# Kernel optimization log

Hardware: AMD Instinct MI355X
Metric: run time of the kernel (lower is better)

The kernel has to match this reference:

```python
import jax, jax.numpy as jnp
import numpy as np

N, E, F, H, O = 50000, 1_600_000, 512, 256, 128


def setup_inputs() -> dict:
    key = jax.random.key(0)
    k1, k2, k3, k4, k5 = jax.random.split(key, 5)
    x = jax.random.normal(k1, (N, F), dtype=jnp.float32)
    edge_index = jax.random.randint(k2, (2, E), 0, N, dtype=jnp.int32)
    edge_weight = jax.random.uniform(k3, (E,), dtype=jnp.float32)
    W1 = jax.random.normal(k4, (F, H), dtype=jnp.float32) * (1.0 / np.sqrt(F))
    b1 = jnp.zeros((H,), dtype=jnp.float32)
    W2 = jax.random.normal(k5, (H, O), dtype=jnp.float32) * (1.0 / np.sqrt(H))
    b2 = jnp.zeros((O,), dtype=jnp.float32)
    return {"x": x, "edge_index": edge_index, "edge_weight": edge_weight,
            "W1": W1, "b1": b1, "W2": W2, "b2": b2}


def reference(x, edge_index, edge_weight, W1, b1, W2, b2):
    n = x.shape[0]
    src, dst = edge_index[0], edge_index[1]
    # GCNConv: add self-loops with weight 1
    loop = jnp.arange(n, dtype=src.dtype)
    src = jnp.concatenate([src, loop])
    dst = jnp.concatenate([dst, loop])
    w = jnp.concatenate([edge_weight, jnp.ones((n,), dtype=x.dtype)])
    # symmetric normalization D^{-1/2} (A+I) D^{-1/2}
    deg = jax.ops.segment_sum(w, dst, num_segments=n)
    dinv = jnp.where(deg > 0, jax.lax.rsqrt(deg), 0.0)
    norm = dinv[src] * w * dinv[dst]  # [E+N]

    def conv(h, W, b):
        h = h @ W                                   # linear first (PyG GCNConv)
        msg = h[src] * norm[:, None]                # gather + scale per edge
        return jax.ops.segment_sum(msg, dst, num_segments=n) + b

    h = jax.nn.relu(conv(x, W1, b1))
    return conv(h, W2, b2)
```

## Files before the change

### kernel.cpp

```cpp
#include <hip/hip_runtime.h>
#include <hip/hip_bf16.h>

#define CAP 80
#define NPB 98
#define BCAP 4096
#define CHUNK_E 2048

typedef __attribute__((ext_vector_type(8))) short bf16x8;
typedef __attribute__((ext_vector_type(4))) float f32x4;
typedef __attribute__((ext_vector_type(2))) float f32x2;

__device__ inline ushort f2bf(float f){
  union{float f; unsigned u;} c{f};
  unsigned r = (c.u + 0x7fff + ((c.u>>16)&1)) >> 16;
  return (ushort)r;
}
__device__ inline float blo(unsigned u){ return __uint_as_float(u<<16); }
__device__ inline float bhi(unsigned u){ return __uint_as_float(u & 0xffff0000u); }


__device__ inline unsigned char fp8_enc(float v){
#if __has_builtin(__builtin_amdgcn_cvt_pk_fp8_f32)
  int p = __builtin_amdgcn_cvt_pk_fp8_f32(v, v, 0, false);
  return (unsigned char)(p & 0xff);
#else
  unsigned s = v < 0.f ? 0x80u : 0u;
  float a = fabsf(v);
  if (a >= 448.f) return (unsigned char)(s | 0x7Eu);
  if (a < 7.8125e-3f){
    int m = (int)rintf(a * 512.f); if (m > 15) m = 15;
    if (m >= 8) return (unsigned char)(s | (1u<<3) | (unsigned)(m-8));
    return (unsigned char)(s | (unsigned)m);
  }
  int e; float fr = frexpf(a, &e);
  int m = (int)rintf(fr * 16.f);
  if (m == 16){ m = 8; e++; }
  int ee = e - 1 + 7;
  if (ee > 15) return (unsigned char)(s | 0x7Eu);
  return (unsigned char)(s | (unsigned)(ee<<3) | (unsigned)(m-8));
#endif
}

__device__ inline void fp8x4_dec(unsigned w, float d[4]){
#if __has_builtin(__builtin_amdgcn_cvt_pk_f32_fp8)
  f32x2 lo = __builtin_amdgcn_cvt_pk_f32_fp8((int)w, false);
  f32x2 hi = __builtin_amdgcn_cvt_pk_f32_fp8((int)w, true);
  d[0] = lo[0]; d[1] = lo[1]; d[2] = hi[0]; d[3] = hi[1];
#else
  #pragma unroll
  for (int i = 0; i < 4; ++i){
    unsigned v = (w >> (8*i)) & 0xffu;
    unsigned s = v & 0x80u, e = (v>>3)&15u, m = v&7u;
    float f = e ? ldexpf((float)(8+m), (int)e - 10) : ldexpf((float)m, -9);
    d[i] = s ? -f : f;
  }
#endif
}


__global__ void k_wconv(const float* __restrict__ Wm, ushort* __restrict__ Wt, int K, int D){
  int idx = blockIdx.x*blockDim.x + threadIdx.x;
  if (idx < D*K){
    int d = idx / K, k = idx - d*K;
    Wt[idx] = f2bf(Wm[(size_t)k*D + d]);
  }
}


__global__ __launch_bounds__(256) void k_bin(const int* __restrict__ src,
                                             const int* __restrict__ dst,
                                             const float* __restrict__ w,
                                             int* __restrict__ bktcur,
                                             uint2* __restrict__ bkt, int E, int nb){
  __shared__ int hist[512];
  __shared__ int base[512];
  const int t  = threadIdx.x;
  const int c0 = blockIdx.x * CHUNK_E;
  const int cend = min(c0 + CHUNK_E, E);
  for (int i = t; i < nb; i += 256) hist[i] = 0;
  __syncthreads();
  const bool full = ((cend - c0) == CHUNK_E) && ((E & 3) == 0);
  int4 d4[2], s4[2]; float4 w4[2];
  if (full){
    const int e0 = c0 + t*8;
    #pragma unroll
    for (int q = 0; q < 2; ++q){
      d4[q] = *(const int4*)(dst + e0 + q*4);
      s4[q] = *(const int4*)(src + e0 + q*4);
      w4[q] = *(const float4*)(w  + e0 + q*4);
    }
    #pragma unroll
    for (int q = 0; q < 2; ++q){
      atomicAdd(&hist[d4[q].x/NPB],1); atomicAdd(&hist[d4[q].y/NPB],1);
      atomicAdd(&hist[d4[q].z/NPB],1); atomicAdd(&hist[d4[q].w/NPB],1);
    }
  } else {
    for (int e = c0 + t; e < cend; e += 256)
      atomicAdd(&hist[dst[e]/NPB], 1);
  }
  __syncthreads();
  for (int i = t; i < nb; i += 256){
    int h = hist[i];
    base[i] = (h > 0) ? atomicAdd(&bktcur[i], h) : 0;
    hist[i] = 0;
  }
  __syncthreads();
  if (full){
    #pragma unroll
    for (int q = 0; q < 2; ++q){
      int   dd[4] = {d4[q].x, d4[q].y, d4[q].z, d4[q].w};
      int   ss[4] = {s4[q].x, s4[q].y, s4[q].z, s4[q].w};
      float ww[4] = {w4[q].x, w4[q].y, w4[q].z, w4[q].w};
      #pragma unroll
      for (int j = 0; j < 4; ++j){
        int b = dd[j] / NPB;
        int pos = base[b] + atomicAdd(&hist[b], 1);
        if (pos < BCAP){
          unsigned lo = ((unsigned)ss[j] << 16) | (unsigned)f2bf(ww[j]);
          bkt[(size_t)b*BCAP + pos] = make_uint2(lo, (unsigned)dd[j]);
        }
      }
    }
  } else {
    for (int e = c0 + t; e < cend; e += 256){
      int d = dst[e];
      int b = d / NPB;
      int pos = base[b] + atomicAdd(&hist[b], 1);
      if (pos < BCAP){
        unsigned lo = ((unsigned)src[e] << 16) | (unsigned)f2bf(w[e]);
        bkt[(size_t)b*BCAP + pos] = make_uint2(lo, (unsigned)d);
      }
    }
  }
}


__global__ __launch_bounds__(256) void k_build(const uint2* __restrict__ bkt,
                                               const int* __restrict__ bktcur,
                                               unsigned* __restrict__ padcsr,
                                               int* __restrict__ cnt,
                                               float* __restrict__ dinv, int N){
  __shared__ unsigned rows[NPB][CAP];
  __shared__ int   lcnt[NPB];
  __shared__ float lws[NPB];
  const int b = blockIdx.x;
  const int t = threadIdx.x;
  const int node0 = b * NPB;
  for (int i = t; i < NPB; i += 256){ lcnt[i] = 0; lws[i] = 0.f; }
  __syncthreads();
  const int cb = min(bktcur[b], BCAP);
  for (int e = t; e < cb; e += 256){
    uint2 rec = bkt[(size_t)b*BCAP + e];
    int ld = (int)rec.y - node0;
    int pos = atomicAdd(&lcnt[ld], 1);
    if (pos < CAP) rows[ld][pos] = rec.x;
    atomicAdd(&lws[ld], blo(rec.x));
  }
  __syncthreads();
  const int maxn = min(NPB, N - node0);
  unsigned* gslice = padcsr + (size_t)node0*CAP;
  const int tot = maxn * CAP;
  const unsigned* lbase = &rows[0][0];
  for (int i = t*4; i < tot; i += 1024)
    *(uint4*)(gslice + i) = *(const uint4*)(lbase + i);
  for (int i = t; i < maxn; i += 256){
    cnt[node0 + i]  = lcnt[i];
    dinv[node0 + i] = rsqrtf(1.f + lws[i]);
  }
}


__global__ __launch_bounds__(256, 3) void gemm1_f8(const float* __restrict__ X,
                                                   const ushort* __restrict__ Wt,
                                                   unsigned char* __restrict__ out, int M){
  __shared__ short As[128][56];
  __shared__ short Bs[256][56];
  const int t    = threadIdx.x;
  const int lane = t & 63;
  const int wave = t >> 6;
  const int wr   = wave >> 1;
  const int wc   = wave & 1;
  const int i0   = blockIdx.x * 128;

  f32x4 acc[4][8];
  #pragma unroll
  for (int m = 0; m < 4; ++m)
    #pragma unroll
    for (int nn = 0; nn < 8; ++nn)
      acc[m][nn] = (f32x4){0.f,0.f,0.f,0.f};

  const int arow = t >> 1;
  const int akh  = (t & 1) * 16;

  for (int kt = 0; kt < 512; kt += 32){
    {
      int gi = i0 + arow;
      ushort hv[16];
      if (gi < M){
        const float4* ap4 = (const float4*)(X + (size_t)gi*512 + kt + akh);
        #pragma unroll
        for (int q = 0; q < 4; ++q){
          float4 v = ap4[q];
          hv[q*4+0] = f2bf(v.x); hv[q*4+1] = f2bf(v.y);
          hv[q*4+2] = f2bf(v.z); hv[q*4+3] = f2bf(v.w);
        }
      } else {
        #pragma unroll
        for (int q = 0; q < 16; ++q) hv[q] = 0;
      }
      *(uint4*)&As[arow][akh]     = *(uint4*)&hv[0];
      *(uint4*)&As[arow][akh + 8] = *(uint4*)&hv[8];
    }
    {
      const ushort* wp = Wt + (size_t)t*512 + kt;
      *(uint4*)&Bs[t][0]  = *(const uint4*)wp;
      *(uint4*)&Bs[t][8]  = *(const uint4*)(wp + 8);
      *(uint4*)&Bs[t][16] = *(const uint4*)(wp + 16);
      *(uint4*)&Bs[t][24] = *(const uint4*)(wp + 24);
    }
    __syncthreads();
    bf16x8 a_f[4], b_f[8];
    #pragma unroll
    for (int m = 0; m < 4; ++m)
      a_f[m] = *(bf16x8*)&As[wr*64 + m*16 + (lane & 15)][(lane >> 4) * 8];
    #pragma unroll
    for (int nn = 0; nn < 8; ++nn)
      b_f[nn] = *(bf16x8*)&Bs[wc*128 + nn*16 + (lane & 15)][(lane >> 4) * 8];
    #pragma unroll
    for (int m = 0; m < 4; ++m)
      #pragma unroll
      for (int nn = 0; nn < 8; ++nn)
        acc[m][nn] = __builtin_amdgcn_mfma_f32_16x16x32_bf16(a_f[m], b_f[nn], acc[m][nn], 0, 0, 0);
    __syncthreads();
  }
  #pragma unroll
  for (int m = 0; m < 4; ++m){
    int r_base = i0 + wr*64 + m*16 + ((lane >> 4) << 2);
    #pragma unroll
    for (int nn = 0; nn < 8; ++nn){
      int c = wc*128 + nn*16 + (lane & 15);
      #pragma unroll
      for (int r = 0; r < 4; ++r){
        int gr = r_base + r;
        if (gr < M) out[(size_t)gr*256 + c] = fp8_enc(acc[m][nn][r]);
      }
    }
  }
}


__global__ __launch_bounds__(256, 2) void gemm2_bf(const ushort* __restrict__ X,
                                                   const ushort* __restrict__ Wt,
                                                   ushort* __restrict__ out, int M){
  constexpr int K = 256, DOUT = 128;
  __shared__ short As[128][56];
  __shared__ short Bs[128][56];
  const int t    = threadIdx.x;
  const int lane = t & 63;
  const int wave = t >> 6;
  const int wr   = wave >> 1;
  const int wc   = wave & 1;
  const int i0   = blockIdx.x * 128;

  f32x4 acc[4][4];
  #pragma unroll
  for (int m = 0; m < 4; ++m)
    #pragma unroll
    for (int nn = 0; nn < 4; ++nn)
      acc[m][nn] = (f32x4){0.f,0.f,0.f,0.f};

  const int arow = t >> 1;
  const int akh  = (t & 1) * 16;

  for (int kt = 0; kt < K; kt += 32){
    {
      int gi = i0 + arow;
      ushort hv[16];
      if (gi < M){
        const uint4* ap4 = (const uint4*)(X + (size_t)gi*K + kt + akh);
        uint4 u0 = ap4[0], u1 = ap4[1];
        *(uint4*)&hv[0] = u0; *(uint4*)&hv[8] = u1;
      } else {
        #pragma unroll
        for (int q = 0; q < 16; ++q) hv[q] = 0;
      }
      *(uint4*)&As[arow][akh]     = *(uint4*)&hv[0];
      *(uint4*)&As[arow][akh + 8] = *(uint4*)&hv[8];
    }
    {
      int bn = t & 127;
      int kh = (t >> 7) * 16;
      const ushort* wp = Wt + (size_t)bn*K + kt + kh;
      *(uint4*)&Bs[bn][kh]     = *(const uint4*)wp;
      *(uint4*)&Bs[bn][kh + 8] = *(const uint4*)(wp + 8);
    }
    __syncthreads();
    bf16x8 a_f[4], b_f[4];
    #pragma unroll
    for (int m = 0; m < 4; ++m)
      a_f[m] = *(bf16x8*)&As[wr*64 + m*16 + (lane & 15)][(lane >> 4) * 8];
    #pragma unroll
    for (int nn = 0; nn < 4; ++nn)
      b_f[nn] = *(bf16x8*)&Bs[wc*64 + nn*16 + (lane & 15)][(lane >> 4) * 8];
    #pragma unroll
    for (int m = 0; m < 4; ++m)
      #pragma unroll
      for (int nn = 0; nn < 4; ++nn)
        acc[m][nn] = __builtin_amdgcn_mfma_f32_16x16x32_bf16(a_f[m], b_f[nn], acc[m][nn], 0, 0, 0);
    __syncthreads();
  }
  #pragma unroll
  for (int m = 0; m < 4; ++m){
    int r_base = i0 + wr*64 + m*16 + ((lane >> 4) << 2);
    #pragma unroll
    for (int nn = 0; nn < 4; ++nn){
      int c = wc*64 + nn*16 + (lane & 15);
      #pragma unroll
      for (int r = 0; r < 4; ++r){
        int gr = r_base + r;
        if (gr < M) out[(size_t)gr*DOUT + c] = f2bf(acc[m][nn][r]);
      }
    }
  }
}


__global__ __launch_bounds__(64) void agg_fp8(const unsigned char* __restrict__ tin,
                                              const int* __restrict__ cnt,
                                              const unsigned* __restrict__ padcsr,
                                              const float* __restrict__ dinv,
                                              const float* __restrict__ bias,
                                              ushort* __restrict__ outp, int n){
  constexpr int U = 4;
  int node = blockIdx.x;
  if (node >= n) return;
  int lane = threadIdx.x & 63;
  int sl   = lane & 15;
  int part = lane >> 4;
  const size_t boff = (size_t)sl * 16;
  const unsigned* row = padcsr + (size_t)node*CAP;

  float acc[16];
  #pragma unroll
  for (int i = 0; i < 16; ++i) acc[i] = 0.f;
  int len = min(cnt[node], CAP);
  int e = 0;
  for (; e + 4*U <= len; e += 4*U){
    int srcs[U]; float ws[U];
    #pragma unroll
    for (int u = 0; u < U; ++u){
      unsigned rec = row[e + u*4 + part];
      srcs[u] = (int)(rec >> 16); ws[u] = blo(rec);
    }
    float dv[U];
    #pragma unroll
    for (int u = 0; u < U; ++u) dv[u] = dinv[srcs[u]];
    uint4 g[U];
    #pragma unroll
    for (int u = 0; u < U; ++u) g[u] = *(const uint4*)(tin + (size_t)srcs[u]*256 + boff);
    #pragma unroll
    for (int u = 0; u < U; ++u){
      float w = ws[u] * dv[u];
      float d[4];
      fp8x4_dec(g[u].x, d);
      acc[0]  += d[0]*w; acc[1]  += d[1]*w; acc[2]  += d[2]*w; acc[3]  += d[3]*w;
      fp8x4_dec(g[u].y, d);
      acc[4]  += d[0]*w; acc[5]  += d[1]*w; acc[6]  += d[2]*w; acc[7]  += d[3]*w;
      fp8x4_dec(g[u].z, d);
      acc[8]  += d[0]*w; acc[9]  += d[1]*w; acc[10] += d[2]*w; acc[11] += d[3]*w;
      fp8x4_dec(g[u].w, d);
      acc[12] += d[0]*w; acc[13] += d[1]*w; acc[14] += d[2]*w; acc[15] += d[3]*w;
    }
  }
  for (; e < len; e += 4){
    int idx = e + part;
    int s = node; float w = 0.f;
    if (idx < len){ unsigned rec = row[idx]; s = (int)(rec >> 16); w = blo(rec) * dinv[s]; }
    uint4 g = *(const uint4*)(tin + (size_t)s*256 + boff);
    float d[4];
    fp8x4_dec(g.x, d);
    acc[0]  += d[0]*w; acc[1]  += d[1]*w; acc[2]  += d[2]*w; acc[3]  += d[3]*w;
    fp8x4_dec(g.y, d);
    acc[4]  += d[0]*w; acc[5]  += d[1]*w; acc[6]  += d[2]*w; acc[7]  += d[3]*w;
    fp8x4_dec(g.z, d);
    acc[8]  += d[0]*w; acc[9]  += d[1]*w; acc[10] += d[2]*w; acc[11] += d[3]*w;
    fp8x4_dec(g.w, d);
    acc[12] += d[0]*w; acc[13] += d[1]*w; acc[14] += d[2]*w; acc[15] += d[3]*w;
  }
  #pragma unroll
  for (int i = 0; i < 16; ++i){
    acc[i] += __shfl_xor(acc[i], 16);
    acc[i] += __shfl_xor(acc[i], 32);
  }
  if (part == 0){
    float di = dinv[node];
    uint4 gs = *(const uint4*)(tin + (size_t)node*256 + boff);
    float d[4];
    fp8x4_dec(gs.x, d);
    acc[0]  += d[0]*di; acc[1]  += d[1]*di; acc[2]  += d[2]*di; acc[3]  += d[3]*di;
    fp8x4_dec(gs.y, d);
    acc[4]  += d[0]*di; acc[5]  += d[1]*di; acc[6]  += d[2]*di; acc[7]  += d[3]*di;
    fp8x4_dec(gs.z, d);
    acc[8]  += d[0]*di; acc[9]  += d[1]*di; acc[10] += d[2]*di; acc[11] += d[3]*di;
    fp8x4_dec(gs.w, d);
    acc[12] += d[0]*di; acc[13] += d[1]*di; acc[14] += d[2]*di; acc[15] += d[3]*di;
    ushort hv[16];
    #pragma unroll
    for (int q = 0; q < 4; ++q){
      float4 bq = *(const float4*)(bias + sl*16 + q*4);
      acc[q*4+0] = acc[q*4+0]*di + bq.x;
      acc[q*4+1] = acc[q*4+1]*di + bq.y;
      acc[q*4+2] = acc[q*4+2]*di + bq.z;
      acc[q*4+3] = acc[q*4+3]*di + bq.w;
    }
    #pragma unroll
    for (int i = 0; i < 16; ++i) hv[i] = f2bf(fmaxf(acc[i], 0.f));
    ushort* op = outp + (size_t)node*256 + sl*16;
    *(uint4*)op       = *(uint4*)&hv[0];
    *(uint4*)(op + 8) = *(uint4*)&hv[8];
  }
}


template<int D, int MODE>
__global__ __launch_bounds__(64) void agg_pad(const ushort* __restrict__ tin,
                                              const int* __restrict__ cnt,
                                              const unsigned* __restrict__ padcsr,
                                              const float* __restrict__ dinv,
                                              const float* __restrict__ bias,
                                              void* __restrict__ outp, int n){
  constexpr int LPR = D/8;
  constexpr int EPW = 64/LPR;
  constexpr int U   = 4;
  int node = blockIdx.x;
  if (node >= n) return;
  int lane = threadIdx.x & 63;
  int sl   = lane & (LPR-1);
  int part = lane / LPR;
  const size_t boff = (size_t)sl*8;
  const unsigned* row = padcsr + (size_t)node*CAP;

  float acc[8] = {0,0,0,0,0,0,0,0};
  int len = min(cnt[node], CAP);
  int e = 0;
  for (; e + EPW*U <= len; e += EPW*U){
    int srcs[U]; float ws[U];
    #pragma unroll
    for (int u = 0; u < U; ++u){
      unsigned rec = row[e + u*EPW + part];
      srcs[u] = (int)(rec >> 16); ws[u] = blo(rec);
    }
    float dv[U];
    #pragma unroll
    for (int u = 0; u < U; ++u) dv[u] = dinv[srcs[u]];
    uint4 g[U];
    #pragma unroll
    for (int u = 0; u < U; ++u) g[u] = *(const uint4*)(tin + (size_t)srcs[u]*D + boff);
    #pragma unroll
    for (int u = 0; u < U; ++u){
      float w = ws[u] * dv[u];
      acc[0] += blo(g[u].x)*w; acc[1] += bhi(g[u].x)*w;
      acc[2] += blo(g[u].y)*w; acc[3] += bhi(g[u].y)*w;
      acc[4] += blo(g[u].z)*w; acc[5] += bhi(g[u].z)*w;
      acc[6] += blo(g[u].w)*w; acc[7] += bhi(g[u].w)*w;
    }
  }
  for (; e < len; e += EPW){
    int idx = e + part;
    int s = node; float w = 0.f;
    if (idx < len){
      unsigned rec = row[idx];
      s = (int)(rec >> 16);
      w = blo(rec) * dinv[s];
    }
    uint4 g = *(const uint4*)(tin + (size_t)s*D + boff);
    acc[0] += blo(g.x)*w; acc[1] += bhi(g.x)*w;
    acc[2] += blo(g.y)*w; acc[3] += bhi(g.y)*w;
    acc[4] += blo(g.z)*w; acc[5] += bhi(g.z)*w;
    acc[6] += blo(g.w)*w; acc[7] += bhi(g.w)*w;
  }
  #pragma unroll
  for (int i = 0; i < 8; ++i){
    if constexpr (EPW == 4) acc[i] += __shfl_xor(acc[i], 16);
    acc[i] += __shfl_xor(acc[i], 32);
  }
  if (part == 0){
    float di = dinv[node];
    uint4 gs = *(const uint4*)(tin + (size_t)node*D + boff);
    acc[0] += blo(gs.x)*di; acc[1] += bhi(gs.x)*di;
    acc[2] += blo(gs.y)*di; acc[3] += bhi(gs.y)*di;
    acc[4] += blo(gs.z)*di; acc[5] += bhi(gs.z)*di;
    acc[6] += blo(gs.w)*di; acc[7] += bhi(gs.w)*di;
    float4 b0 = *(const float4*)(bias + sl*8);
    float4 b1 = *(const float4*)(bias + sl*8 + 4);
    acc[0] = acc[0]*di + b0.x; acc[1] = acc[1]*di + b0.y;
    acc[2] = acc[2]*di + b0.z; acc[3] = acc[3]*di + b0.w;
    acc[4] = acc[4]*di + b1.x; acc[5] = acc[5]*di + b1.y;
    acc[6] = acc[6]*di + b1.z; acc[7] = acc[7]*di + b1.w;
    if constexpr (MODE == 0){
      ushort hv[8];
      #pragma unroll
      for (int i = 0; i < 8; ++i) hv[i] = f2bf(fmaxf(acc[i], 0.f));
      *(uint4*)((ushort*)outp + (size_t)node*D + boff) = *(uint4*)&hv[0];
    } else {
      float* op = (float*)outp + (size_t)node*D + boff;
      *(float4*)op     = make_float4(acc[0],acc[1],acc[2],acc[3]);
      *(float4*)(op+4) = make_float4(acc[4],acc[5],acc[6],acc[7]);
    }
  }
}


static inline size_t align_up(size_t x){ return (x + 255) & ~(size_t)255; }

extern "C" void kernel_launch(void* const* d_in, const int* in_sizes, int n_in,
                              void* d_out, int out_size, void* d_ws, size_t ws_size,
                              hipStream_t stream){
  const float* x   = (const float*)d_in[0];
  const int*   ei  = (const int*)  d_in[1];
  const float* ew  = (const float*)d_in[2];
  const float* W1  = (const float*)d_in[3];
  const float* b1  = (const float*)d_in[4];
  const float* W2  = (const float*)d_in[5];
  const float* b2  = (const float*)d_in[6];

  const int H = in_sizes[4];
  const int F = in_sizes[3] / H;
  const int N = in_sizes[0] / F;
  const int E = in_sizes[2];
  const int O = in_sizes[6];

  const int* src = ei;
  const int* dst = ei + E;

  const int nb = (N + NPB - 1) / NPB;

  char* p = (char*)d_ws;
  int*      cnt     = (int*)p;            p += align_up((size_t)N*4);
  float*    dinv    = (float*)p;          p += align_up((size_t)N*4);
  int*      bktcur  = (int*)p;            p += align_up((size_t)nb*4);
  ushort*   Wt1     = (ushort*)p;         p += align_up((size_t)H*F*2);
  ushort*   Wt2     = (ushort*)p;         p += align_up((size_t)O*H*2);
  unsigned* padcsr  = (unsigned*)p;       p += align_up((size_t)N*CAP*4);
  unsigned char* t1 = (unsigned char*)p;  p += align_up((size_t)N*H);
  uint2*    bkt     = (uint2*)p;
  ushort*   h1      = (ushort*)p;         p += align_up((size_t)N*H*2 > (size_t)nb*BCAP*8 ?
                                                        (size_t)N*H*2 : (size_t)nb*BCAP*8);
  ushort*   t2      = (ushort*)t1;

  hipLaunchKernelGGL(k_wconv, dim3((H*F+255)/256), dim3(256), 0, stream, W1, Wt1, F, H);
  hipLaunchKernelGGL(k_wconv, dim3((O*H+255)/256), dim3(256), 0, stream, W2, Wt2, H, O);

  hipMemsetAsync(bktcur, 0, (size_t)nb*4, stream);
  hipLaunchKernelGGL(k_bin, dim3((E+CHUNK_E-1)/CHUNK_E), dim3(256), 0, stream,
                     src, dst, ew, bktcur, bkt, E, nb);
  hipLaunchKernelGGL(k_build, dim3(nb), dim3(256), 0, stream,
                     bkt, bktcur, padcsr, cnt, dinv, N);

  hipLaunchKernelGGL(gemm1_f8, dim3((N+127)/128), dim3(256), 0, stream, x, Wt1, t1, N);
  hipLaunchKernelGGL(agg_fp8, dim3(N), dim3(64), 0, stream,
                     t1, cnt, padcsr, dinv, b1, h1, N);

  hipLaunchKernelGGL(gemm2_bf, dim3((N+127)/128), dim3(256), 0, stream, h1, Wt2, t2, N);
  hipLaunchKernelGGL((agg_pad<128,1>), dim3(N), dim3(64), 0, stream,
                     t2, cnt, padcsr, dinv, b2, d_out, N);
}
```

Measured before the change: 235.5 us.

## Merge weight conversion into binning kernel and shrink GEMM row tiles to 64

Folds the two weight-transpose/bf16 conversion launches into the edge-binning kernel as extra leading blocks, removing two kernel launches. Both GEMMs move from 128-row to 64-row tiles with fewer accumulators per wave and higher launch-bounds occupancy, giving more blocks across the GPU for N=50000. The B-tile load in gemm1 is staggered to reduce LDS bank conflicts. Smaller tiles reload the weight tile more often per output row, which raises global and LDS traffic.

```diff
diff --git a/kernel.cpp b/kernel.cpp
--- a/kernel.cpp
+++ b/kernel.cpp
@@ -58,24 +58,32 @@
 }
 
 
-__global__ void k_wconv(const float* __restrict__ Wm, ushort* __restrict__ Wt, int K, int D){
-  int idx = blockIdx.x*blockDim.x + threadIdx.x;
-  if (idx < D*K){
-    int d = idx / K, k = idx - d*K;
-    Wt[idx] = f2bf(Wm[(size_t)k*D + d]);
-  }
-}
-
-
-__global__ __launch_bounds__(256) void k_bin(const int* __restrict__ src,
-                                             const int* __restrict__ dst,
+__global__ __launch_bounds__(256) void k_pre(const float* __restrict__ W1, ushort* __restrict__ Wt1,
+                                             const float* __restrict__ W2, ushort* __restrict__ Wt2,
+                                             const int* __restrict__ src, const int* __restrict__ dst,
                                              const float* __restrict__ w,
-                                             int* __restrict__ bktcur,
-                                             uint2* __restrict__ bkt, int E, int nb){
+                                             int* __restrict__ bktcur, uint2* __restrict__ bkt,
+                                             int E, int nb, int gb, int F, int H, int O){
+  const int t = threadIdx.x;
+  if ((int)blockIdx.x < gb){
+    int idx = blockIdx.x*256 + t;
+    int n1 = H*F;
+    if (idx < n1){
+      int d = idx / F, k = idx - d*F;
+      Wt1[idx] = f2bf(W1[(size_t)k*H + d]);
+    } else {
+      int j = idx - n1;
+      if (j < O*H){
+        int d = j / H, k = j - d*H;
+        Wt2[j] = f2bf(W2[(size_t)k*O + d]);
+      }
+    }
+    return;
+  }
   __shared__ int hist[512];
   __shared__ int base[512];
-  const int t  = threadIdx.x;
-  const int c0 = blockIdx.x * CHUNK_E;
+  const int bb = blockIdx.x - gb;
+  const int c0 = bb * CHUNK_E;
   const int cend = min(c0 + CHUNK_E, E);
   for (int i = t; i < nb; i += 256) hist[i] = 0;
   __syncthreads();
@@ -170,75 +178,70 @@
 }
 
 
-__global__ __launch_bounds__(256, 3) void gemm1_f8(const float* __restrict__ X,
+__global__ __launch_bounds__(256, 4) void gemm1_f8(const float* __restrict__ X,
                                                    const ushort* __restrict__ Wt,
                                                    unsigned char* __restrict__ out, int M){
-  __shared__ short As[128][56];
+  __shared__ short As[64][56];
   __shared__ short Bs[256][56];
   const int t    = threadIdx.x;
   const int lane = t & 63;
   const int wave = t >> 6;
-  const int wr   = wave >> 1;
-  const int wc   = wave & 1;
-  const int i0   = blockIdx.x * 128;
-
-  f32x4 acc[4][8];
+  const int i0   = blockIdx.x * 64;
+
+  f32x4 acc[4][4];
   #pragma unroll
   for (int m = 0; m < 4; ++m)
     #pragma unroll
-    for (int nn = 0; nn < 8; ++nn)
+    for (int nn = 0; nn < 4; ++nn)
       acc[m][nn] = (f32x4){0.f,0.f,0.f,0.f};
 
-  const int arow = t >> 1;
-  const int akh  = (t & 1) * 16;
+  const int arow = t >> 2;
+  const int ak8  = (t & 3) * 8;
 
   for (int kt = 0; kt < 512; kt += 32){
     {
       int gi = i0 + arow;
-      ushort hv[16];
+      ushort hv[8];
       if (gi < M){
-        const float4* ap4 = (const float4*)(X + (size_t)gi*512 + kt + akh);
-        #pragma unroll
-        for (int q = 0; q < 4; ++q){
-          float4 v = ap4[q];
-          hv[q*4+0] = f2bf(v.x); hv[q*4+1] = f2bf(v.y);
-          hv[q*4+2] = f2bf(v.z); hv[q*4+3] = f2bf(v.w);
-        }
+        const float4* ap4 = (const float4*)(X + (size_t)gi*512 + kt + ak8);
+        float4 v0 = ap4[0], v1 = ap4[1];
+        hv[0]=f2bf(v0.x); hv[1]=f2bf(v0.y); hv[2]=f2bf(v0.z); hv[3]=f2bf(v0.w);
+        hv[4]=f2bf(v1.x); hv[5]=f2bf(v1.y); hv[6]=f2bf(v1.z); hv[7]=f2bf(v1.w);
       } else {
         #pragma unroll
-        for (int q = 0; q < 16; ++q) hv[q] = 0;
-      }
-      *(uint4*)&As[arow][akh]     = *(uint4*)&hv[0];
-      *(uint4*)&As[arow][akh + 8] = *(uint4*)&hv[8];
+        for (int q = 0; q < 8; ++q) hv[q] = 0;
+      }
+      *(uint4*)&As[arow][ak8] = *(uint4*)&hv[0];
     }
     {
       const ushort* wp = Wt + (size_t)t*512 + kt;
-      *(uint4*)&Bs[t][0]  = *(const uint4*)wp;
-      *(uint4*)&Bs[t][8]  = *(const uint4*)(wp + 8);
-      *(uint4*)&Bs[t][16] = *(const uint4*)(wp + 16);
-      *(uint4*)&Bs[t][24] = *(const uint4*)(wp + 24);
+      #pragma unroll
+      for (int k = 0; k < 4; ++k){
+        int g = (k + (t >> 1)) & 3;
+        *(uint4*)&Bs[t][g*8] = *(const uint4*)(wp + g*8);
+      }
     }
     __syncthreads();
-    bf16x8 a_f[4], b_f[8];
+    bf16x8 a_f[4], b_f[4];
     #pragma unroll
     for (int m = 0; m < 4; ++m)
-      a_f[m] = *(bf16x8*)&As[wr*64 + m*16 + (lane & 15)][(lane >> 4) * 8];
-    #pragma unroll
-    for (int nn = 0; nn < 8; ++nn)
-      b_f[nn] = *(bf16x8*)&Bs[wc*128 + nn*16 + (lane & 15)][(lane >> 4) * 8];
+      a_f[m] = *(bf16x8*)&As[m*16 + (lane & 15)][(lane >> 4) * 8];
+    #pragma unroll
+    for (int nn = 0; nn < 4; ++nn)
+      b_f[nn] = *(bf16x8*)&Bs[wave*64 + nn*16 + (lane & 15)][(lane >> 4) * 8];
     #pragma unroll
     for (int m = 0; m < 4; ++m)
       #pragma unroll
-      for (int nn = 0; nn < 8; ++nn)
+      for (int nn = 0; nn < 4; ++nn)
         acc[m][nn] = __builtin_amdgcn_mfma_f32_16x16x32_bf16(a_f[m], b_f[nn], acc[m][nn], 0, 0, 0);
     __syncthreads();
   }
   #pragma unroll
   for (int m = 0; m < 4; ++m){
-    int r_base = i0 + wr*64 + m*16 + ((lane >> 4) << 2);
-    #pragma unroll
-    for (int nn = 0; nn < 8; ++nn){
-      int c = wc*128 + nn*16 + (lane & 15);
+    int r_base = i0 + m*16 + ((lane >> 4) << 2);
+    #pragma unroll
+    for (int nn = 0; nn < 4; ++nn){
+      int c = wave*64 + nn*16 + (lane & 15);
       #pragma unroll
       for (int r = 0; r < 4; ++r){
         int gr = r_base + r;
@@ -249,69 +252,64 @@
 }
 
 
-__global__ __launch_bounds__(256, 2) void gemm2_bf(const ushort* __restrict__ X,
+__global__ __launch_bounds__(256, 4) void gemm2_bf(const ushort* __restrict__ X,
                                                    const ushort* __restrict__ Wt,
                                                    ushort* __restrict__ out, int M){
   constexpr int K = 256, DOUT = 128;
-  __shared__ short As[128][56];
+  __shared__ short As[64][56];
   __shared__ short Bs[128][56];
   const int t    = threadIdx.x;
   const int lane = t & 63;
   const int wave = t >> 6;
   const int wr   = wave >> 1;
   const int wc   = wave & 1;
-  const int i0   = blockIdx.x * 128;
-
-  f32x4 acc[4][4];
-  #pragma unroll
-  for (int m = 0; m < 4; ++m)
+  const int i0   = blockIdx.x * 64;
+
+  f32x4 acc[2][4];
+  #pragma unroll
+  for (int m = 0; m < 2; ++m)
     #pragma unroll
     for (int nn = 0; nn < 4; ++nn)
       acc[m][nn] = (f32x4){0.f,0.f,0.f,0.f};
 
-  const int arow = t >> 1;
-  const int akh  = (t & 1) * 16;
+  const int arow = t >> 2;
+  const int ak8  = (t & 3) * 8;
 
   for (int kt = 0; kt < K; kt += 32){
     {
       int gi = i0 + arow;
-      ushort hv[16];
       if (gi < M){
-        const uint4* ap4 = (const uint4*)(X + (size_t)gi*K + kt + akh);
-        uint4 u0 = ap4[0], u1 = ap4[1];
-        *(uint4*)&hv[0] = u0; *(uint4*)&hv[8] = u1;
+        *(uint4*)&As[arow][ak8] = *(const uint4*)(X + (size_t)gi*K + kt + ak8);
       } else {
-        #pragma unroll
-        for (int q = 0; q < 16; ++q) hv[q] = 0;
-      }
-      *(uint4*)&As[arow][akh]     = *(uint4*)&hv[0];
-      *(uint4*)&As[arow][akh + 8] = *(uint4*)&hv[8];
+        uint4 z = {0,0,0,0};
+        *(uint4*)&As[arow][ak8] = z;
+      }
     }
     {
-      int bn = t & 127;
-      int kh = (t >> 7) * 16;
+      int bn = t >> 1;
+      int kh = (t & 1) * 16;
       const ushort* wp = Wt + (size_t)bn*K + kt + kh;
       *(uint4*)&Bs[bn][kh]     = *(const uint4*)wp;
       *(uint4*)&Bs[bn][kh + 8] = *(const uint4*)(wp + 8);
     }
     __syncthreads();
-    bf16x8 a_f[4], b_f[4];
-    #pragma unroll
-    for (int m = 0; m < 4; ++m)
-      a_f[m] = *(bf16x8*)&As[wr*64 + m*16 + (lane & 15)][(lane >> 4) * 8];
+    bf16x8 a_f[2], b_f[4];
+    #pragma unroll
+    for (int m = 0; m < 2; ++m)
+      a_f[m] = *(bf16x8*)&As[wr*32 + m*16 + (lane & 15)][(lane >> 4) * 8];
     #pragma unroll
     for (int nn = 0; nn < 4; ++nn)
       b_f[nn] = *(bf16x8*)&Bs[wc*64 + nn*16 + (lane & 15)][(lane >> 4) * 8];
     #pragma unroll
-    for (int m = 0; m < 4; ++m)
+    for (int m = 0; m < 2; ++m)
       #pragma unroll
       for (int nn = 0; nn < 4; ++nn)
         acc[m][nn] = __builtin_amdgcn_mfma_f32_16x16x32_bf16(a_f[m], b_f[nn], acc[m][nn], 0, 0, 0);
     __syncthreads();
   }
   #pragma unroll
-  for (int m = 0; m < 4; ++m){
-    int r_base = i0 + wr*64 + m*16 + ((lane >> 4) << 2);
+  for (int m = 0; m < 2; ++m){
+    int r_base = i0 + wr*32 + m*16 + ((lane >> 4) << 2);
     #pragma unroll
     for (int nn = 0; nn < 4; ++nn){
       int c = wc*64 + nn*16 + (lane & 15);
@@ -534,6 +532,8 @@
   const int* dst = ei + E;
 
   const int nb = (N + NPB - 1) / NPB;
+  const int gb = (H*F + O*H + 255) / 256;
+  const int binb = (E + CHUNK_E - 1) / CHUNK_E;
 
   char* p = (char*)d_ws;
   int*      cnt     = (int*)p;            p += align_up((size_t)N*4);
@@ -548,20 +548,17 @@
                                                         (size_t)N*H*2 : (size_t)nb*BCAP*8);
   ushort*   t2      = (ushort*)t1;
 
-  hipLaunchKernelGGL(k_wconv, dim3((H*F+255)/256), dim3(256), 0, stream, W1, Wt1, F, H);
-  hipLaunchKernelGGL(k_wconv, dim3((O*H+255)/256), dim3(256), 0, stream, W2, Wt2, H, O);
-
   hipMemsetAsync(bktcur, 0, (size_t)nb*4, stream);
-  hipLaunchKernelGGL(k_bin, dim3((E+CHUNK_E-1)/CHUNK_E), dim3(256), 0, stream,
-                     src, dst, ew, bktcur, bkt, E, nb);
+  hipLaunchKernelGGL(k_pre, dim3(gb + binb), dim3(256), 0, stream,
+                     W1, Wt1, W2, Wt2, src, dst, ew, bktcur, bkt, E, nb, gb, F, H, O);
   hipLaunchKernelGGL(k_build, dim3(nb), dim3(256), 0, stream,
                      bkt, bktcur, padcsr, cnt, dinv, N);
 
-  hipLaunchKernelGGL(gemm1_f8, dim3((N+127)/128), dim3(256), 0, stream, x, Wt1, t1, N);
+  hipLaunchKernelGGL(gemm1_f8, dim3((N+63)/64), dim3(256), 0, stream, x, Wt1, t1, N);
   hipLaunchKernelGGL(agg_fp8, dim3(N), dim3(64), 0, stream,
                      t1, cnt, padcsr, dinv, b1, h1, N);
 
-  hipLaunchKernelGGL(gemm2_bf, dim3((N+127)/128), dim3(256), 0, stream, h1, Wt2, t2, N);
+  hipLaunchKernelGGL(gemm2_bf, dim3((N+63)/64), dim3(256), 0, stream, h1, Wt2, t2, N);
   hipLaunchKernelGGL((agg_pad<128,1>), dim3(N), dim3(64), 0, stream,
                      t2, cnt, padcsr, dinv, b2, d_out, N);
 }
```

Measured after the change: 220.5 us, median of 2. 1.07x faster.
